# Kernel optimization log

Measured on AMD Instinct MI355X. Metric: run time of the kernel, lower is better.

## Reference

```python
import jax, jax.numpy as jnp
import numpy as np

N = 100000   # nodes
E = 1600000  # directed edges (avg degree 16)
D = 128      # num_feature == hidden_channels


def setup_inputs() -> dict:
    key = jax.random.key(0)
    ks = jax.random.split(key, 8)
    s = 1.0 / np.sqrt(D)
    x = jax.random.normal(ks[0], (N, D), jnp.float32)
    edge_index = jax.random.randint(ks[1], (2, E), 0, N, dtype=jnp.int32)
    W1 = jax.random.normal(ks[2], (D, D), jnp.float32) * s
    W2 = jax.random.normal(ks[3], (D, D), jnp.float32) * s
    W3 = jax.random.normal(ks[4], (D, D), jnp.float32) * s
    b1 = jnp.zeros((D,), jnp.float32)
    b2 = jnp.zeros((D,), jnp.float32)
    b3 = jnp.zeros((D,), jnp.float32)
    return {"x": x, "edge_index": edge_index, "W1": W1, "b1": b1,
            "W2": W2, "b2": b2, "W3": W3, "b3": b3}


def reference(x, edge_index, W1, b1, W2, b2, W3, b3):
    # GCNConv with added self-loops and symmetric normalization:
    #   out = D^{-1/2} (A + I) D^{-1/2} (x W) + b
    loops = jnp.arange(N, dtype=edge_index.dtype)
    src = jnp.concatenate([edge_index[0], loops])  # [E+N]
    dst = jnp.concatenate([edge_index[1], loops])
    deg = jax.ops.segment_sum(jnp.ones_like(dst, x.dtype), dst, num_segments=N)
    dinv = jax.lax.rsqrt(deg)                      # deg >= 1 (self-loops)
    norm = dinv[src] * dinv[dst]                   # [E+N]

    def conv(h, W, b):
        h = h @ W                                   # [N, D] dense GEMM
        msg = h[src] * norm[:, None]                # gather + scale [E+N, D]
        return jax.ops.segment_sum(msg, dst, num_segments=N) + b

    # dropout is identity in eval mode
    h = jax.nn.relu(conv(x, W1, b1))
    h = jax.nn.relu(conv(h, W2, b2))
    return conv(h, W3, b3)
```

## Files before the change

### kernel.cpp

```cpp
#include <hip/hip_runtime.h>
#include <hip/hip_fp16.h>

#define DFEAT 128
#define BNODES 256
#define BSHIFT 8
#define B1CHUNK 4096
#define SLABC 8192
#define TPB_TILES 2

typedef _Float16 f16x8 __attribute__((ext_vector_type(8)));
typedef _Float16 f16x4 __attribute__((ext_vector_type(4)));
typedef float f32x4 __attribute__((ext_vector_type(4)));


__global__ __launch_bounds__(256) void bin_k(const int* __restrict__ src, const int* __restrict__ dst,
                                             int* __restrict__ gcnt, unsigned int* __restrict__ slab,
                                             int E, int nbuck) {
    __shared__ int cnt[512];
    __shared__ int off[512];
    __shared__ int gbase[512];
    __shared__ int sd[256];
    __shared__ unsigned int buf[B1CHUNK];
    __shared__ unsigned short bid[B1CHUNK];
    int t = threadIdx.x;
    int base = blockIdx.x * B1CHUNK;
    int nloc = E - base;
    if (nloc > B1CHUNK) nloc = B1CHUNK;
    cnt[t] = 0;
    cnt[t + 256] = 0;
    __syncthreads();
    int k = t;
    for (; k + 768 < nloc; k += 1024) {
        int d0 = dst[base + k], d1 = dst[base + k + 256], d2 = dst[base + k + 512], d3 = dst[base + k + 768];
        atomicAdd(&cnt[d0 >> BSHIFT], 1);
        atomicAdd(&cnt[d1 >> BSHIFT], 1);
        atomicAdd(&cnt[d2 >> BSHIFT], 1);
        atomicAdd(&cnt[d3 >> BSHIFT], 1);
    }
    for (; k < nloc; k += 256) atomicAdd(&cnt[dst[base + k] >> BSHIFT], 1);
    __syncthreads();
    int v0 = cnt[2 * t], v1 = cnt[2 * t + 1];
    int tsum = v0 + v1;
    sd[t] = tsum;
    __syncthreads();
    for (int o = 1; o < 256; o <<= 1) {
        int x = (t >= o) ? sd[t - o] : 0;
        __syncthreads();
        sd[t] += x;
        __syncthreads();
    }
    int texcl = sd[t] - tsum;
    off[2 * t] = texcl;
    off[2 * t + 1] = texcl + v0;
    if (2 * t < nbuck && v0 > 0) gbase[2 * t] = atomicAdd(&gcnt[2 * t], v0);
    if (2 * t + 1 < nbuck && v1 > 0) gbase[2 * t + 1] = atomicAdd(&gcnt[2 * t + 1], v1);
    __syncthreads();
    k = t;
    for (; k + 768 < nloc; k += 1024) {
        int d0 = dst[base + k], d1 = dst[base + k + 256], d2 = dst[base + k + 512], d3 = dst[base + k + 768];
        int s0 = src[base + k], s1 = src[base + k + 256], s2 = src[base + k + 512], s3 = src[base + k + 768];
        int b0 = d0 >> BSHIFT, b1_ = d1 >> BSHIFT, b2_ = d2 >> BSHIFT, b3_ = d3 >> BSHIFT;
        int r0 = atomicAdd(&off[b0], 1); buf[r0] = ((unsigned)s0 << BSHIFT) | (unsigned)(d0 & (BNODES - 1)); bid[r0] = (unsigned short)b0;
        int r1 = atomicAdd(&off[b1_], 1); buf[r1] = ((unsigned)s1 << BSHIFT) | (unsigned)(d1 & (BNODES - 1)); bid[r1] = (unsigned short)b1_;
        int r2 = atomicAdd(&off[b2_], 1); buf[r2] = ((unsigned)s2 << BSHIFT) | (unsigned)(d2 & (BNODES - 1)); bid[r2] = (unsigned short)b2_;
        int r3 = atomicAdd(&off[b3_], 1); buf[r3] = ((unsigned)s3 << BSHIFT) | (unsigned)(d3 & (BNODES - 1)); bid[r3] = (unsigned short)b3_;
    }
    for (; k < nloc; k += 256) {
        int d = dst[base + k];
        int s = src[base + k];
        int b = d >> BSHIFT;
        int r = atomicAdd(&off[b], 1);
        buf[r] = ((unsigned)s << BSHIFT) | (unsigned)(d & (BNODES - 1));
        bid[r] = (unsigned short)b;
    }
    __syncthreads();
    k = t;
    for (; k + 768 < nloc; k += 1024) {
#pragma unroll
        for (int u = 0; u < 4; ++u) {
            int kk = k + u * 256;
            int b = bid[kk];
            int o0 = off[b] - cnt[b];
            int pos = gbase[b] + (kk - o0);
            if (pos < SLABC) slab[(size_t)b * SLABC + pos] = buf[kk];
        }
    }
    for (; k < nloc; k += 256) {
        int b = bid[k];
        int o0 = off[b] - cnt[b];
        int pos = gbase[b] + (k - o0);
        if (pos < SLABC) slab[(size_t)b * SLABC + pos] = buf[k];
    }
}

__global__ __launch_bounds__(256) void bucketAB_k(const unsigned int* __restrict__ slab,
                                                  const int* __restrict__ gcnt,
                                                  int* __restrict__ rp, float* __restrict__ dinv,
                                                  int* __restrict__ cols, int N, int nbuck) {
    __shared__ int cnt[256];
    __shared__ int cur[256];
    __shared__ int psum[256];
    __shared__ int outb[SLABC];
    int t = threadIdx.x;
    int b = blockIdx.x;
    int n0 = b << BSHIFT;
    int nn = N - n0;
    if (nn > BNODES) nn = BNODES;
    int ne_raw = gcnt[b];
    int ne = ne_raw > SLABC ? SLABC : ne_raw;
    const unsigned int* sl = slab + (size_t)b * SLABC;
    int part = 0;
    for (int i = t; i < b; i += 256) part += gcnt[i];
    psum[t] = part;
    cnt[t] = 0;
    __syncthreads();
    for (int o = 128; o > 0; o >>= 1) {
        if (t < o) psum[t] += psum[t + o];
        __syncthreads();
    }
    int base = psum[0];
    int k = t;
    for (; k + 768 < ne; k += 1024) {
        unsigned a0 = sl[k], a1 = sl[k + 256], a2 = sl[k + 512], a3 = sl[k + 768];
        atomicAdd(&cnt[a0 & (BNODES - 1)], 1);
        atomicAdd(&cnt[a1 & (BNODES - 1)], 1);
        atomicAdd(&cnt[a2 & (BNODES - 1)], 1);
        atomicAdd(&cnt[a3 & (BNODES - 1)], 1);
    }
    for (; k < ne; k += 256) atomicAdd(&cnt[sl[k] & (BNODES - 1)], 1);
    __syncthreads();
    int deg = cnt[t];
    for (int o = 1; o < 256; o <<= 1) {
        int x = (t >= o) ? cnt[t - o] : 0;
        __syncthreads();
        cnt[t] += x;
        __syncthreads();
    }
    int excl = cnt[t] - deg;
    if (t < nn) {
        rp[n0 + t] = base + excl;
        dinv[n0 + t] = rsqrtf((float)(deg + 1));
    }
    if (b == nbuck - 1 && t == 0) rp[N] = base + ne_raw;
    cur[t] = excl;
    __syncthreads();
    k = t;
    for (; k + 768 < ne; k += 1024) {
        unsigned a0 = sl[k], a1 = sl[k + 256], a2 = sl[k + 512], a3 = sl[k + 768];
        int p0 = atomicAdd(&cur[a0 & (BNODES - 1)], 1); outb[p0] = (int)(a0 >> BSHIFT);
        int p1 = atomicAdd(&cur[a1 & (BNODES - 1)], 1); outb[p1] = (int)(a1 >> BSHIFT);
        int p2 = atomicAdd(&cur[a2 & (BNODES - 1)], 1); outb[p2] = (int)(a2 >> BSHIFT);
        int p3 = atomicAdd(&cur[a3 & (BNODES - 1)], 1); outb[p3] = (int)(a3 >> BSHIFT);
    }
    for (; k < ne; k += 256) {
        unsigned a = sl[k];
        int p = atomicAdd(&cur[a & (BNODES - 1)], 1);
        outb[p] = (int)(a >> BSHIFT);
    }
    __syncthreads();
    k = t;
    for (; k + 768 < ne; k += 1024) {
        int o0 = outb[k], o1 = outb[k + 256], o2 = outb[k + 512], o3 = outb[k + 768];
        cols[base + k] = o0;
        cols[base + k + 256] = o1;
        cols[base + k + 512] = o2;
        cols[base + k + 768] = o3;
    }
    for (; k < ne; k += 256) cols[base + k] = outb[k];
}

__global__ __launch_bounds__(256) void packW_k(const float* __restrict__ W0, const float* __restrict__ W1,
                                               const float* __restrict__ W2,
                                               const float* __restrict__ b0, const float* __restrict__ b1,
                                               const float* __restrict__ b2,
                                               _Float16* __restrict__ wpk, float* __restrict__ bp,
                                               int* __restrict__ gcnt) {
    int idx = blockIdx.x * 256 + threadIdx.x;
    int layer = idx >> 14;
    int e = idx & 16383;
    int k = e >> 7;
    int nn = e & 127;
    const float* W = (layer == 0) ? W0 : ((layer == 1) ? W1 : W2);
    int ksrc = (layer == 0) ? k : (((k & 7) << 4) | (k >> 3));
    float v = W[ksrc * DFEAT + nn];
    int kc = k >> 5, quad = (k >> 3) & 3, j = k & 7;
    int ct = nn >> 4;
    int pos = ((ct * 4 + kc) * 64 + quad * 16 + (nn & 15)) * 8 + j;
    wpk[(size_t)layer * 16384 + pos] = (_Float16)v;
    if (idx < 384) {
        int l = idx >> 7, p = idx & 127;
        int c = ((p & 7) << 4) | (p >> 3);
        const float* bb = (l == 0) ? b0 : ((l == 1) ? b1 : b2);
        bp[l * 128 + p] = bb[c];
    }
    if (idx < 512) gcnt[idx] = 0;
}


__device__ inline f16x8 ldA8(const float* p) {
    float4 a = *(const float4*)p;
    float4 b = *(const float4*)(p + 4);
    return f16x8{(_Float16)a.x, (_Float16)a.y, (_Float16)a.z, (_Float16)a.w,
                 (_Float16)b.x, (_Float16)b.y, (_Float16)b.z, (_Float16)b.w};
}
__device__ inline f16x8 ldA8(const __half* p) { return *(const f16x8*)p; }
__device__ inline f16x8 zero8() {
    return f16x8{(_Float16)0.f, (_Float16)0.f, (_Float16)0.f, (_Float16)0.f,
                 (_Float16)0.f, (_Float16)0.f, (_Float16)0.f, (_Float16)0.f};
}

template <typename TIN>
__global__ __launch_bounds__(256) void gemmP_k(const TIN* __restrict__ A, const _Float16* __restrict__ wfrag,
                                               const float* __restrict__ dinv, __half* __restrict__ C,
                                               int n, int ntiles) {
    __shared__ _Float16 al[8192];
    __shared__ _Float16 wl[16384];
    const int tid = threadIdx.x;
    const int wv_ = tid >> 6;
    const int lane = tid & 63;
    const int t0 = blockIdx.x * TPB_TILES;
    const int chunk = tid & 15;
    const int rsub = tid >> 4;
    const int kcS = chunk >> 2, quadS = chunk & 3;
    const int swzS = (kcS << 1) ^ (quadS & 1);

    for (int c = tid; c < 2048; c += 256)
        *(f16x8*)&wl[c * 8] = *(const f16x8*)&wfrag[c * 8];

    f16x8 pre[4];
    {
        int row0 = t0 * 64;
#pragma unroll
        for (int p = 0; p < 4; ++p) {
            int gr = row0 + p * 16 + rsub;
            pre[p] = (gr < n) ? ldA8(&A[(size_t)gr * DFEAT + chunk * 8]) : zero8();
        }
    }
    for (int tt = 0; tt < TPB_TILES; ++tt) {
        int tile = t0 + tt;
        if (tile >= ntiles) break;
        int row0 = tile * 64;
#pragma unroll
        for (int p = 0; p < 4; ++p) {
            int idx = (p * 4 + kcS) * 64 + quadS * 16 + rsub;
            *(f16x8*)&al[(idx ^ swzS) * 8] = pre[p];
        }
        __syncthreads();
        if (tt + 1 < TPB_TILES && tile + 1 < ntiles) {
            int nrow0 = (tile + 1) * 64;
#pragma unroll
            for (int p = 0; p < 4; ++p) {
                int gr = nrow0 + p * 16 + rsub;
                pre[p] = (gr < n) ? ldA8(&A[(size_t)gr * DFEAT + chunk * 8]) : zero8();
            }
        }
        f16x8 af[4];
        const int swzR = (lane >> 4) & 1;
#pragma unroll
        for (int kc = 0; kc < 4; ++kc) {
            int idx = (wv_ * 4 + kc) * 64 + lane;
            af[kc] = *(f16x8*)&al[(idx ^ (kc << 1) ^ swzR) * 8];
        }
        const int quad = lane >> 4, cb = lane & 15;
        const int rbase = row0 + wv_ * 16 + quad * 4;
        float ds[4];
#pragma unroll
        for (int r = 0; r < 4; ++r) ds[r] = (rbase + r < n) ? dinv[rbase + r] : 0.f;
        f32x4 acc[8];
#pragma unroll
        for (int ct = 0; ct < 8; ++ct) acc[ct] = (f32x4){0.f, 0.f, 0.f, 0.f};
#pragma unroll
        for (int ct = 0; ct < 8; ++ct) {
#pragma unroll
            for (int kc = 0; kc < 4; ++kc) {
                f16x8 bf = *(f16x8*)&wl[((ct * 4 + kc) * 64 + lane) * 8];
                acc[ct] = __builtin_amdgcn_mfma_f32_16x16x32_f16(af[kc], bf, acc[ct], 0, 0, 0);
            }
        }
#pragma unroll
        for (int r = 0; r < 4; ++r) {
            int gr = rbase + r;
            if (gr < n) {
                f16x8 o;
#pragma unroll
                for (int ct = 0; ct < 8; ++ct) o[ct] = (_Float16)(acc[ct][r] * ds[r]);
                *(f16x8*)&C[(size_t)gr * DFEAT + cb * 8] = o;
            }
        }
        __syncthreads();
    }
}


__device__ inline float2 agg_row(const __half* __restrict__ T, const int* __restrict__ rowptr,
                                 const int* __restrict__ cols, int wid, int lane, int fb) {
    float2 t0 = __half22float2(*(const __half2*)(T + (size_t)wid * DFEAT + fb));
    float ax = t0.x;
    float ay = t0.y;
    int s = rowptr[wid], e = rowptr[wid + 1];
    for (int p = s; p < e; ) {
        int take = e - p;
        if (take > 64) take = 64;
        int q = p + lane;
        if (q >= e) q = e - 1;
        int ci = cols[q];
        int j = 0;
        for (; j + 8 <= take; j += 8) {
            int c0 = __builtin_amdgcn_readlane(ci, j + 0);
            int c1 = __builtin_amdgcn_readlane(ci, j + 1);
            int c2 = __builtin_amdgcn_readlane(ci, j + 2);
            int c3 = __builtin_amdgcn_readlane(ci, j + 3);
            int c4 = __builtin_amdgcn_readlane(ci, j + 4);
            int c5 = __builtin_amdgcn_readlane(ci, j + 5);
            int c6 = __builtin_amdgcn_readlane(ci, j + 6);
            int c7 = __builtin_amdgcn_readlane(ci, j + 7);
            float2 v0 = __half22float2(*(const __half2*)(T + (size_t)c0 * DFEAT + fb));
            float2 v1 = __half22float2(*(const __half2*)(T + (size_t)c1 * DFEAT + fb));
            float2 v2 = __half22float2(*(const __half2*)(T + (size_t)c2 * DFEAT + fb));
            float2 v3 = __half22float2(*(const __half2*)(T + (size_t)c3 * DFEAT + fb));
            float2 v4 = __half22float2(*(const __half2*)(T + (size_t)c4 * DFEAT + fb));
            float2 v5 = __half22float2(*(const __half2*)(T + (size_t)c5 * DFEAT + fb));
            float2 v6 = __half22float2(*(const __half2*)(T + (size_t)c6 * DFEAT + fb));
            float2 v7 = __half22float2(*(const __half2*)(T + (size_t)c7 * DFEAT + fb));
            ax += v0.x; ay += v0.y;
            ax += v1.x; ay += v1.y;
            ax += v2.x; ay += v2.y;
            ax += v3.x; ay += v3.y;
            ax += v4.x; ay += v4.y;
            ax += v5.x; ay += v5.y;
            ax += v6.x; ay += v6.y;
            ax += v7.x; ay += v7.y;
        }
        for (; j < take; ++j) {
            int c = __builtin_amdgcn_readlane(ci, j);
            float2 v = __half22float2(*(const __half2*)(T + (size_t)c * DFEAT + fb));
            ax += v.x; ay += v.y;
        }
        p += take;
    }
    return make_float2(ax, ay);
}

__global__ __launch_bounds__(256) void agg_k(const __half* __restrict__ T, const float* __restrict__ dinv,
                                             const int* __restrict__ rowptr, const int* __restrict__ cols,
                                             const float* __restrict__ biasp,
                                             __half* __restrict__ out, int n) {
    int wid = (int)((blockIdx.x * (size_t)blockDim.x + threadIdx.x) >> 6);
    int lane = threadIdx.x & 63;
    if (wid >= n) return;
    int fb = lane * 2;
    float2 a = agg_row(T, rowptr, cols, wid, lane, fb);
    float dw = dinv[wid];
    float ox = fmaxf(dw * a.x + biasp[fb], 0.f);
    float oy = fmaxf(dw * a.y + biasp[fb + 1], 0.f);
    *(__half2*)(out + (size_t)wid * DFEAT + fb) = __floats2half2_rn(ox, oy);
}

__global__ __launch_bounds__(256) void aggF_k(const __half* __restrict__ T, const float* __restrict__ dinv,
                                              const int* __restrict__ rowptr, const int* __restrict__ cols,
                                              const float* __restrict__ biasp,
                                              float* __restrict__ out, int n) {
    int wid = (int)((blockIdx.x * (size_t)blockDim.x + threadIdx.x) >> 6);
    int lane = threadIdx.x & 63;
    if (wid >= n) return;
    int fb = lane * 2;
    float2 a = agg_row(T, rowptr, cols, wid, lane, fb);
    float dw = dinv[wid];
    float ox = dw * a.x + biasp[fb];
    float oy = dw * a.y + biasp[fb + 1];
    int c0 = ((fb & 7) << 4) | (fb >> 3);
    int c1 = (((fb + 1) & 7) << 4) | ((fb + 1) >> 3);
    out[(size_t)wid * DFEAT + c0] = ox;
    out[(size_t)wid * DFEAT + c1] = oy;
}


extern "C" void kernel_launch(void* const* d_in, const int* in_sizes, int n_in,
                              void* d_out, int out_size, void* d_ws, size_t ws_size,
                              hipStream_t stream) {
    const float* x  = (const float*)d_in[0];
    const int*   ei = (const int*)d_in[1];
    const float* W1 = (const float*)d_in[2];
    const float* b1 = (const float*)d_in[3];
    const float* W2 = (const float*)d_in[4];
    const float* b2 = (const float*)d_in[5];
    const float* W3 = (const float*)d_in[6];
    const float* b3 = (const float*)d_in[7];
    float* out = (float*)d_out;

    const int N = in_sizes[0] / DFEAT;
    const int E = in_sizes[1] / 2;
    const int* srcp = ei;
    const int* dstp = ei + E;

    size_t off = 0;
    auto alloc = [&](size_t bytes) -> void* {
        void* p = (char*)d_ws + off;
        off += (bytes + 255) & ~(size_t)255;
        return p;
    };
    const int nbuck = (N + BNODES - 1) / BNODES;

    int*    gcnt = (int*)alloc(2048);
    int*    rp   = (int*)alloc((size_t)(N + 1) * 4);
    float*  dinv = (float*)alloc((size_t)N * 4);
    _Float16* wpk = (_Float16*)alloc((size_t)3 * 16384 * 2);
    float*  bp   = (float*)alloc(3 * 128 * 4);
    unsigned int* slab = (unsigned int*)alloc((size_t)nbuck * SLABC * 4);
    int*    cols = (int*)alloc((size_t)E * 4);
    __half* bufA = (__half*)alloc((size_t)N * DFEAT * 2);
    __half* bufB = (__half*)alloc((size_t)N * DFEAT * 2);

    packW_k<<<192, 256, 0, stream>>>(W1, W2, W3, b1, b2, b3, wpk, bp, gcnt);
    bin_k<<<(E + B1CHUNK - 1) / B1CHUNK, 256, 0, stream>>>(srcp, dstp, gcnt, slab, E, nbuck);
    bucketAB_k<<<nbuck, 256, 0, stream>>>(slab, gcnt, rp, dinv, cols, N, nbuck);

    int ntiles = (N + 63) / 64;
    int gemmGrid = (ntiles + TPB_TILES - 1) / TPB_TILES;
    int aggGrid  = (int)(((size_t)N * 64 + 255) / 256);

    gemmP_k<float><<<gemmGrid, 256, 0, stream>>>(x, wpk, dinv, bufA, N, ntiles);
    agg_k<<<aggGrid, 256, 0, stream>>>(bufA, dinv, rp, cols, bp, bufB, N);

    gemmP_k<__half><<<gemmGrid, 256, 0, stream>>>(bufB, wpk + 16384, dinv, bufA, N, ntiles);
    agg_k<<<aggGrid, 256, 0, stream>>>(bufA, dinv, rp, cols, bp + 128, bufB, N);

    gemmP_k<__half><<<gemmGrid, 256, 0, stream>>>(bufB, wpk + 32768, dinv, bufA, N, ntiles);
    aggF_k<<<aggGrid, 256, 0, stream>>>(bufA, dinv, rp, cols, bp + 256, out, N);
}
```

Baseline: 379.4 us.

## Fuse edge binning with first-layer GEMM and apply source norm during aggregation

The edge-binning kernel and the layer-1 dense GEMM now run in one launch, with block ranges split between the two jobs, so the GEMM work overlaps the atomic-heavy binning. This is possible because the first GEMM no longer scales rows by dinv, which is not yet computed at that point. A new aggregation kernel applies dinv of each source node per edge instead. The cost is an extra dinv gather per edge in the first aggregation, plus shared memory sized for the larger of the two roles.

```diff
diff --git a/kernel.cpp b/kernel.cpp
--- a/kernel.cpp
+++ b/kernel.cpp
@@ -7,167 +7,12 @@
 #define B1CHUNK 4096
 #define SLABC 8192
 #define TPB_TILES 2
+#define TPB1 2
 
 typedef _Float16 f16x8 __attribute__((ext_vector_type(8)));
 typedef _Float16 f16x4 __attribute__((ext_vector_type(4)));
 typedef float f32x4 __attribute__((ext_vector_type(4)));
 
-
-__global__ __launch_bounds__(256) void bin_k(const int* __restrict__ src, const int* __restrict__ dst,
-                                             int* __restrict__ gcnt, unsigned int* __restrict__ slab,
-                                             int E, int nbuck) {
-    __shared__ int cnt[512];
-    __shared__ int off[512];
-    __shared__ int gbase[512];
-    __shared__ int sd[256];
-    __shared__ unsigned int buf[B1CHUNK];
-    __shared__ unsigned short bid[B1CHUNK];
-    int t = threadIdx.x;
-    int base = blockIdx.x * B1CHUNK;
-    int nloc = E - base;
-    if (nloc > B1CHUNK) nloc = B1CHUNK;
-    cnt[t] = 0;
-    cnt[t + 256] = 0;
-    __syncthreads();
-    int k = t;
-    for (; k + 768 < nloc; k += 1024) {
-        int d0 = dst[base + k], d1 = dst[base + k + 256], d2 = dst[base + k + 512], d3 = dst[base + k + 768];
-        atomicAdd(&cnt[d0 >> BSHIFT], 1);
-        atomicAdd(&cnt[d1 >> BSHIFT], 1);
-        atomicAdd(&cnt[d2 >> BSHIFT], 1);
-        atomicAdd(&cnt[d3 >> BSHIFT], 1);
-    }
-    for (; k < nloc; k += 256) atomicAdd(&cnt[dst[base + k] >> BSHIFT], 1);
-    __syncthreads();
-    int v0 = cnt[2 * t], v1 = cnt[2 * t + 1];
-    int tsum = v0 + v1;
-    sd[t] = tsum;
-    __syncthreads();
-    for (int o = 1; o < 256; o <<= 1) {
-        int x = (t >= o) ? sd[t - o] : 0;
-        __syncthreads();
-        sd[t] += x;
-        __syncthreads();
-    }
-    int texcl = sd[t] - tsum;
-    off[2 * t] = texcl;
-    off[2 * t + 1] = texcl + v0;
-    if (2 * t < nbuck && v0 > 0) gbase[2 * t] = atomicAdd(&gcnt[2 * t], v0);
-    if (2 * t + 1 < nbuck && v1 > 0) gbase[2 * t + 1] = atomicAdd(&gcnt[2 * t + 1], v1);
-    __syncthreads();
-    k = t;
-    for (; k + 768 < nloc; k += 1024) {
-        int d0 = dst[base + k], d1 = dst[base + k + 256], d2 = dst[base + k + 512], d3 = dst[base + k + 768];
-        int s0 = src[base + k], s1 = src[base + k + 256], s2 = src[base + k + 512], s3 = src[base + k + 768];
-        int b0 = d0 >> BSHIFT, b1_ = d1 >> BSHIFT, b2_ = d2 >> BSHIFT, b3_ = d3 >> BSHIFT;
-        int r0 = atomicAdd(&off[b0], 1); buf[r0] = ((unsigned)s0 << BSHIFT) | (unsigned)(d0 & (BNODES - 1)); bid[r0] = (unsigned short)b0;
-        int r1 = atomicAdd(&off[b1_], 1); buf[r1] = ((unsigned)s1 << BSHIFT) | (unsigned)(d1 & (BNODES - 1)); bid[r1] = (unsigned short)b1_;
-        int r2 = atomicAdd(&off[b2_], 1); buf[r2] = ((unsigned)s2 << BSHIFT) | (unsigned)(d2 & (BNODES - 1)); bid[r2] = (unsigned short)b2_;
-        int r3 = atomicAdd(&off[b3_], 1); buf[r3] = ((unsigned)s3 << BSHIFT) | (unsigned)(d3 & (BNODES - 1)); bid[r3] = (unsigned short)b3_;
-    }
-    for (; k < nloc; k += 256) {
-        int d = dst[base + k];
-        int s = src[base + k];
-        int b = d >> BSHIFT;
-        int r = atomicAdd(&off[b], 1);
-        buf[r] = ((unsigned)s << BSHIFT) | (unsigned)(d & (BNODES - 1));
-        bid[r] = (unsigned short)b;
-    }
-    __syncthreads();
-    k = t;
-    for (; k + 768 < nloc; k += 1024) {
-#pragma unroll
-        for (int u = 0; u < 4; ++u) {
-            int kk = k + u * 256;
-            int b = bid[kk];
-            int o0 = off[b] - cnt[b];
-            int pos = gbase[b] + (kk - o0);
-            if (pos < SLABC) slab[(size_t)b * SLABC + pos] = buf[kk];
-        }
-    }
-    for (; k < nloc; k += 256) {
-        int b = bid[k];
-        int o0 = off[b] - cnt[b];
-        int pos = gbase[b] + (k - o0);
-        if (pos < SLABC) slab[(size_t)b * SLABC + pos] = buf[k];
-    }
-}
-
-__global__ __launch_bounds__(256) void bucketAB_k(const unsigned int* __restrict__ slab,
-                                                  const int* __restrict__ gcnt,
-                                                  int* __restrict__ rp, float* __restrict__ dinv,
-                                                  int* __restrict__ cols, int N, int nbuck) {
-    __shared__ int cnt[256];
-    __shared__ int cur[256];
-    __shared__ int psum[256];
-    __shared__ int outb[SLABC];
-    int t = threadIdx.x;
-    int b = blockIdx.x;
-    int n0 = b << BSHIFT;
-    int nn = N - n0;
-    if (nn > BNODES) nn = BNODES;
-    int ne_raw = gcnt[b];
-    int ne = ne_raw > SLABC ? SLABC : ne_raw;
-    const unsigned int* sl = slab + (size_t)b * SLABC;
-    int part = 0;
-    for (int i = t; i < b; i += 256) part += gcnt[i];
-    psum[t] = part;
-    cnt[t] = 0;
-    __syncthreads();
-    for (int o = 128; o > 0; o >>= 1) {
-        if (t < o) psum[t] += psum[t + o];
-        __syncthreads();
-    }
-    int base = psum[0];
-    int k = t;
-    for (; k + 768 < ne; k += 1024) {
-        unsigned a0 = sl[k], a1 = sl[k + 256], a2 = sl[k + 512], a3 = sl[k + 768];
-        atomicAdd(&cnt[a0 & (BNODES - 1)], 1);
-        atomicAdd(&cnt[a1 & (BNODES - 1)], 1);
-        atomicAdd(&cnt[a2 & (BNODES - 1)], 1);
-        atomicAdd(&cnt[a3 & (BNODES - 1)], 1);
-    }
-    for (; k < ne; k += 256) atomicAdd(&cnt[sl[k] & (BNODES - 1)], 1);
-    __syncthreads();
-    int deg = cnt[t];
-    for (int o = 1; o < 256; o <<= 1) {
-        int x = (t >= o) ? cnt[t - o] : 0;
-        __syncthreads();
-        cnt[t] += x;
-        __syncthreads();
-    }
-    int excl = cnt[t] - deg;
-    if (t < nn) {
-        rp[n0 + t] = base + excl;
-        dinv[n0 + t] = rsqrtf((float)(deg + 1));
-    }
-    if (b == nbuck - 1 && t == 0) rp[N] = base + ne_raw;
-    cur[t] = excl;
-    __syncthreads();
-    k = t;
-    for (; k + 768 < ne; k += 1024) {
-        unsigned a0 = sl[k], a1 = sl[k + 256], a2 = sl[k + 512], a3 = sl[k + 768];
-        int p0 = atomicAdd(&cur[a0 & (BNODES - 1)], 1); outb[p0] = (int)(a0 >> BSHIFT);
-        int p1 = atomicAdd(&cur[a1 & (BNODES - 1)], 1); outb[p1] = (int)(a1 >> BSHIFT);
-        int p2 = atomicAdd(&cur[a2 & (BNODES - 1)], 1); outb[p2] = (int)(a2 >> BSHIFT);
-        int p3 = atomicAdd(&cur[a3 & (BNODES - 1)], 1); outb[p3] = (int)(a3 >> BSHIFT);
-    }
-    for (; k < ne; k += 256) {
-        unsigned a = sl[k];
-        int p = atomicAdd(&cur[a & (BNODES - 1)], 1);
-        outb[p] = (int)(a >> BSHIFT);
-    }
-    __syncthreads();
-    k = t;
-    for (; k + 768 < ne; k += 1024) {
-        int o0 = outb[k], o1 = outb[k + 256], o2 = outb[k + 512], o3 = outb[k + 768];
-        cols[base + k] = o0;
-        cols[base + k + 256] = o1;
-        cols[base + k + 512] = o2;
-        cols[base + k + 768] = o3;
-    }
-    for (; k < ne; k += 256) cols[base + k] = outb[k];
-}
 
 __global__ __launch_bounds__(256) void packW_k(const float* __restrict__ W0, const float* __restrict__ W1,
                                                const float* __restrict__ W2,
@@ -196,7 +41,6 @@
     if (idx < 512) gcnt[idx] = 0;
 }
 
-
 __device__ inline f16x8 ldA8(const float* p) {
     float4 a = *(const float4*)p;
     float4 b = *(const float4*)(p + 4);
@@ -207,6 +51,221 @@
 __device__ inline f16x8 zero8() {
     return f16x8{(_Float16)0.f, (_Float16)0.f, (_Float16)0.f, (_Float16)0.f,
                  (_Float16)0.f, (_Float16)0.f, (_Float16)0.f, (_Float16)0.f};
+}
+
+struct BinSh {
+    int cnt[512];
+    int off[512];
+    int gbase[512];
+    int sd[256];
+    unsigned int buf[B1CHUNK];
+    unsigned short bid[B1CHUNK];
+};
+struct G1Sh {
+    _Float16 wl[16384];
+};
+
+__global__ __launch_bounds__(256) void binGemm1_k(const int* __restrict__ src, const int* __restrict__ dst,
+                                                  int* __restrict__ gcnt, unsigned int* __restrict__ slab,
+                                                  int E, int nbuck, int nbin,
+                                                  const float* __restrict__ A, const _Float16* __restrict__ wfrag,
+                                                  __half* __restrict__ C, int n, int ntiles) {
+    __shared__ __align__(16) char smem[32768];
+    int t = threadIdx.x;
+    if (blockIdx.x >= nbin) {
+        _Float16* wl = ((G1Sh*)smem)->wl;
+        const int wv_ = t >> 6;
+        const int lane = t & 63;
+        const int m = lane & 15;
+        const int q = lane >> 4;
+        for (int c = t; c < 2048; c += 256)
+            *(f16x8*)&wl[c * 8] = *(const f16x8*)&wfrag[c * 8];
+        __syncthreads();
+        int t0 = (blockIdx.x - nbin) * TPB1;
+        int tend = t0 + TPB1;
+        if (tend > ntiles) tend = ntiles;
+        for (int tile = t0; tile < tend; ++tile) {
+            int row0 = tile * 64;
+            int ga = row0 + wv_ * 16 + m;
+            f16x8 af[4];
+            if (ga < n) {
+#pragma unroll
+                for (int kc = 0; kc < 4; ++kc)
+                    af[kc] = ldA8(&A[(size_t)ga * DFEAT + kc * 32 + q * 8]);
+            } else {
+#pragma unroll
+                for (int kc = 0; kc < 4; ++kc) af[kc] = zero8();
+            }
+            f32x4 acc[8];
+#pragma unroll
+            for (int ct = 0; ct < 8; ++ct) acc[ct] = (f32x4){0.f, 0.f, 0.f, 0.f};
+#pragma unroll
+            for (int ct = 0; ct < 8; ++ct) {
+#pragma unroll
+                for (int kc = 0; kc < 4; ++kc) {
+                    f16x8 bf = *(f16x8*)&wl[((ct * 4 + kc) * 64 + lane) * 8];
+                    acc[ct] = __builtin_amdgcn_mfma_f32_16x16x32_f16(af[kc], bf, acc[ct], 0, 0, 0);
+                }
+            }
+            const int rbase = row0 + wv_ * 16 + q * 4;
+#pragma unroll
+            for (int r = 0; r < 4; ++r) {
+                int gr = rbase + r;
+                if (gr < n) {
+                    f16x8 o;
+#pragma unroll
+                    for (int ct = 0; ct < 8; ++ct) o[ct] = (_Float16)acc[ct][r];
+                    *(f16x8*)&C[(size_t)gr * DFEAT + m * 8] = o;
+                }
+            }
+        }
+        return;
+    }
+    BinSh* B = (BinSh*)smem;
+    int base = blockIdx.x * B1CHUNK;
+    int nloc = E - base;
+    if (nloc > B1CHUNK) nloc = B1CHUNK;
+    B->cnt[t] = 0;
+    B->cnt[t + 256] = 0;
+    __syncthreads();
+    int k = t;
+    for (; k + 768 < nloc; k += 1024) {
+        int d0 = dst[base + k], d1 = dst[base + k + 256], d2 = dst[base + k + 512], d3 = dst[base + k + 768];
+        atomicAdd(&B->cnt[d0 >> BSHIFT], 1);
+        atomicAdd(&B->cnt[d1 >> BSHIFT], 1);
+        atomicAdd(&B->cnt[d2 >> BSHIFT], 1);
+        atomicAdd(&B->cnt[d3 >> BSHIFT], 1);
+    }
+    for (; k < nloc; k += 256) atomicAdd(&B->cnt[dst[base + k] >> BSHIFT], 1);
+    __syncthreads();
+    int v0 = B->cnt[2 * t], v1 = B->cnt[2 * t + 1];
+    int tsum = v0 + v1;
+    B->sd[t] = tsum;
+    __syncthreads();
+    for (int o = 1; o < 256; o <<= 1) {
+        int x = (t >= o) ? B->sd[t - o] : 0;
+        __syncthreads();
+        B->sd[t] += x;
+        __syncthreads();
+    }
+    int texcl = B->sd[t] - tsum;
+    B->off[2 * t] = texcl;
+    B->off[2 * t + 1] = texcl + v0;
+    if (2 * t < nbuck && v0 > 0) B->gbase[2 * t] = atomicAdd(&gcnt[2 * t], v0);
+    if (2 * t + 1 < nbuck && v1 > 0) B->gbase[2 * t + 1] = atomicAdd(&gcnt[2 * t + 1], v1);
+    __syncthreads();
+    k = t;
+    for (; k + 768 < nloc; k += 1024) {
+        int d0 = dst[base + k], d1 = dst[base + k + 256], d2 = dst[base + k + 512], d3 = dst[base + k + 768];
+        int s0 = src[base + k], s1 = src[base + k + 256], s2 = src[base + k + 512], s3 = src[base + k + 768];
+        int b0_ = d0 >> BSHIFT, b1_ = d1 >> BSHIFT, b2_ = d2 >> BSHIFT, b3_ = d3 >> BSHIFT;
+        int r0 = atomicAdd(&B->off[b0_], 1); B->buf[r0] = ((unsigned)s0 << BSHIFT) | (unsigned)(d0 & (BNODES - 1)); B->bid[r0] = (unsigned short)b0_;
+        int r1 = atomicAdd(&B->off[b1_], 1); B->buf[r1] = ((unsigned)s1 << BSHIFT) | (unsigned)(d1 & (BNODES - 1)); B->bid[r1] = (unsigned short)b1_;
+        int r2 = atomicAdd(&B->off[b2_], 1); B->buf[r2] = ((unsigned)s2 << BSHIFT) | (unsigned)(d2 & (BNODES - 1)); B->bid[r2] = (unsigned short)b2_;
+        int r3 = atomicAdd(&B->off[b3_], 1); B->buf[r3] = ((unsigned)s3 << BSHIFT) | (unsigned)(d3 & (BNODES - 1)); B->bid[r3] = (unsigned short)b3_;
+    }
+    for (; k < nloc; k += 256) {
+        int d = dst[base + k];
+        int s = src[base + k];
+        int b = d >> BSHIFT;
+        int r = atomicAdd(&B->off[b], 1);
+        B->buf[r] = ((unsigned)s << BSHIFT) | (unsigned)(d & (BNODES - 1));
+        B->bid[r] = (unsigned short)b;
+    }
+    __syncthreads();
+    k = t;
+    for (; k + 768 < nloc; k += 1024) {
+#pragma unroll
+        for (int u = 0; u < 4; ++u) {
+            int kk = k + u * 256;
+            int b = B->bid[kk];
+            int o0 = B->off[b] - B->cnt[b];
+            int pos = B->gbase[b] + (kk - o0);
+            if (pos < SLABC) slab[(size_t)b * SLABC + pos] = B->buf[kk];
+        }
+    }
+    for (; k < nloc; k += 256) {
+        int b = B->bid[k];
+        int o0 = B->off[b] - B->cnt[b];
+        int pos = B->gbase[b] + (k - o0);
+        if (pos < SLABC) slab[(size_t)b * SLABC + pos] = B->buf[k];
+    }
+}
+
+__global__ __launch_bounds__(256) void bucketAB_k(const unsigned int* __restrict__ slab,
+                                                  const int* __restrict__ gcnt,
+                                                  int* __restrict__ rp, float* __restrict__ dinv,
+                                                  int* __restrict__ cols, int N, int nbuck) {
+    __shared__ int cnt[256];
+    __shared__ int cur[256];
+    __shared__ int psum[256];
+    __shared__ int outb[SLABC];
+    int t = threadIdx.x;
+    int b = blockIdx.x;
+    int n0 = b << BSHIFT;
+    int nn = N - n0;
+    if (nn > BNODES) nn = BNODES;
+    int ne_raw = gcnt[b];
+    int ne = ne_raw > SLABC ? SLABC : ne_raw;
+    const unsigned int* sl = slab + (size_t)b * SLABC;
+    int part = 0;
+    for (int i = t; i < b; i += 256) part += gcnt[i];
+    psum[t] = part;
+    cnt[t] = 0;
+    __syncthreads();
+    for (int o = 128; o > 0; o >>= 1) {
+        if (t < o) psum[t] += psum[t + o];
+        __syncthreads();
+    }
+    int base = psum[0];
+    int k = t;
+    for (; k + 768 < ne; k += 1024) {
+        unsigned a0 = sl[k], a1 = sl[k + 256], a2 = sl[k + 512], a3 = sl[k + 768];
+        atomicAdd(&cnt[a0 & (BNODES - 1)], 1);
+        atomicAdd(&cnt[a1 & (BNODES - 1)], 1);
+        atomicAdd(&cnt[a2 & (BNODES - 1)], 1);
+        atomicAdd(&cnt[a3 & (BNODES - 1)], 1);
+    }
+    for (; k < ne; k += 256) atomicAdd(&cnt[sl[k] & (BNODES - 1)], 1);
+    __syncthreads();
+    int deg = cnt[t];
+    for (int o = 1; o < 256; o <<= 1) {
+        int x = (t >= o) ? cnt[t - o] : 0;
+        __syncthreads();
+        cnt[t] += x;
+        __syncthreads();
+    }
+    int excl = cnt[t] - deg;
+    if (t < nn) {
+        rp[n0 + t] = base + excl;
+        dinv[n0 + t] = rsqrtf((float)(deg + 1));
+    }
+    if (b == nbuck - 1 && t == 0) rp[N] = base + ne_raw;
+    cur[t] = excl;
+    __syncthreads();
+    k = t;
+    for (; k + 768 < ne; k += 1024) {
+        unsigned a0 = sl[k], a1 = sl[k + 256], a2 = sl[k + 512], a3 = sl[k + 768];
+        int p0 = atomicAdd(&cur[a0 & (BNODES - 1)], 1); outb[p0] = (int)(a0 >> BSHIFT);
+        int p1 = atomicAdd(&cur[a1 & (BNODES - 1)], 1); outb[p1] = (int)(a1 >> BSHIFT);
+        int p2 = atomicAdd(&cur[a2 & (BNODES - 1)], 1); outb[p2] = (int)(a2 >> BSHIFT);
+        int p3 = atomicAdd(&cur[a3 & (BNODES - 1)], 1); outb[p3] = (int)(a3 >> BSHIFT);
+    }
+    for (; k < ne; k += 256) {
+        unsigned a = sl[k];
+        int p = atomicAdd(&cur[a & (BNODES - 1)], 1);
+        outb[p] = (int)(a >> BSHIFT);
+    }
+    __syncthreads();
+    k = t;
+    for (; k + 768 < ne; k += 1024) {
+        int o0 = outb[k], o1 = outb[k + 256], o2 = outb[k + 512], o3 = outb[k + 768];
+        cols[base + k] = o0;
+        cols[base + k + 256] = o1;
+        cols[base + k + 512] = o2;
+        cols[base + k + 768] = o3;
+    }
+    for (; k < ne; k += 256) cols[base + k] = outb[k];
 }
 
 template <typename TIN>
@@ -291,6 +350,67 @@
     }
 }
 
+
+__global__ __launch_bounds__(256) void aggW_k(const __half* __restrict__ T, const float* __restrict__ dinv,
+                                              const int* __restrict__ rowptr, const int* __restrict__ cols,
+                                              const float* __restrict__ biasp,
+                                              __half* __restrict__ out, int n) {
+    int wid = (int)((blockIdx.x * (size_t)blockDim.x + threadIdx.x) >> 6);
+    int lane = threadIdx.x & 63;
+    if (wid >= n) return;
+    int fb = lane * 2;
+    float di = dinv[wid];
+    float2 t0 = __half22float2(*(const __half2*)(T + (size_t)wid * DFEAT + fb));
+    float ax = di * t0.x;
+    float ay = di * t0.y;
+    int s = rowptr[wid], e = rowptr[wid + 1];
+    for (int p = s; p < e; ) {
+        int take = e - p;
+        if (take > 64) take = 64;
+        int q = p + lane;
+        if (q >= e) q = e - 1;
+        int ci = cols[q];
+        int j = 0;
+        for (; j + 8 <= take; j += 8) {
+            int c0 = __builtin_amdgcn_readlane(ci, j + 0);
+            int c1 = __builtin_amdgcn_readlane(ci, j + 1);
+            int c2 = __builtin_amdgcn_readlane(ci, j + 2);
+            int c3 = __builtin_amdgcn_readlane(ci, j + 3);
+            int c4 = __builtin_amdgcn_readlane(ci, j + 4);
+            int c5 = __builtin_amdgcn_readlane(ci, j + 5);
+            int c6 = __builtin_amdgcn_readlane(ci, j + 6);
+            int c7 = __builtin_amdgcn_readlane(ci, j + 7);
+            float w0 = dinv[c0], w1 = dinv[c1], w2 = dinv[c2], w3 = dinv[c3];
+            float w4 = dinv[c4], w5 = dinv[c5], w6 = dinv[c6], w7 = dinv[c7];
+            float2 v0 = __half22float2(*(const __half2*)(T + (size_t)c0 * DFEAT + fb));
+            float2 v1 = __half22float2(*(const __half2*)(T + (size_t)c1 * DFEAT + fb));
+            float2 v2 = __half22float2(*(const __half2*)(T + (size_t)c2 * DFEAT + fb));
+            float2 v3 = __half22float2(*(const __half2*)(T + (size_t)c3 * DFEAT + fb));
+            float2 v4 = __half22float2(*(const __half2*)(T + (size_t)c4 * DFEAT + fb));
+            float2 v5 = __half22float2(*(const __half2*)(T + (size_t)c5 * DFEAT + fb));
+            float2 v6 = __half22float2(*(const __half2*)(T + (size_t)c6 * DFEAT + fb));
+            float2 v7 = __half22float2(*(const __half2*)(T + (size_t)c7 * DFEAT + fb));
+            ax += w0 * v0.x; ay += w0 * v0.y;
+            ax += w1 * v1.x; ay += w1 * v1.y;
+            ax += w2 * v2.x; ay += w2 * v2.y;
+            ax += w3 * v3.x; ay += w3 * v3.y;
+            ax += w4 * v4.x; ay += w4 * v4.y;
+            ax += w5 * v5.x; ay += w5 * v5.y;
+            ax += w6 * v6.x; ay += w6 * v6.y;
+            ax += w7 * v7.x; ay += w7 * v7.y;
+        }
+        for (; j < take; ++j) {
+            int c = __builtin_amdgcn_readlane(ci, j);
+            float w = dinv[c];
+            float2 v = __half22float2(*(const __half2*)(T + (size_t)c * DFEAT + fb));
+            ax += w * v.x; ay += w * v.y;
+        }
+        p += take;
+    }
+    float ox = fmaxf(di * ax + biasp[fb], 0.f);
+    float oy = fmaxf(di * ay + biasp[fb + 1], 0.f);
+    *(__half2*)(out + (size_t)wid * DFEAT + fb) = __floats2half2_rn(ox, oy);
+}
 
 __device__ inline float2 agg_row(const __half* __restrict__ T, const int* __restrict__ rowptr,
                                  const int* __restrict__ cols, int wid, int lane, int fb) {
@@ -411,16 +531,18 @@
     __half* bufA = (__half*)alloc((size_t)N * DFEAT * 2);
     __half* bufB = (__half*)alloc((size_t)N * DFEAT * 2);
 
-    packW_k<<<192, 256, 0, stream>>>(W1, W2, W3, b1, b2, b3, wpk, bp, gcnt);
-    bin_k<<<(E + B1CHUNK - 1) / B1CHUNK, 256, 0, stream>>>(srcp, dstp, gcnt, slab, E, nbuck);
-    bucketAB_k<<<nbuck, 256, 0, stream>>>(slab, gcnt, rp, dinv, cols, N, nbuck);
-
+    const int nbin = (E + B1CHUNK - 1) / B1CHUNK;
     int ntiles = (N + 63) / 64;
+    int g1blocks = (ntiles + TPB1 - 1) / TPB1;
     int gemmGrid = (ntiles + TPB_TILES - 1) / TPB_TILES;
     int aggGrid  = (int)(((size_t)N * 64 + 255) / 256);
 
-    gemmP_k<float><<<gemmGrid, 256, 0, stream>>>(x, wpk, dinv, bufA, N, ntiles);
-    agg_k<<<aggGrid, 256, 0, stream>>>(bufA, dinv, rp, cols, bp, bufB, N);
+    packW_k<<<192, 256, 0, stream>>>(W1, W2, W3, b1, b2, b3, wpk, bp, gcnt);
+    binGemm1_k<<<nbin + g1blocks, 256, 0, stream>>>(srcp, dstp, gcnt, slab, E, nbuck, nbin,
+                                                    x, wpk, bufA, N, ntiles);
+    bucketAB_k<<<nbuck, 256, 0, stream>>>(slab, gcnt, rp, dinv, cols, N, nbuck);
+
+    aggW_k<<<aggGrid, 256, 0, stream>>>(bufA, dinv, rp, cols, bp, bufB, N);
 
     gemmP_k<__half><<<gemmGrid, 256, 0, stream>>>(bufB, wpk + 16384, dinv, bufA, N, ntiles);
     agg_k<<<aggGrid, 256, 0, stream>>>(bufA, dinv, rp, cols, bp + 128, bufB, N);
```

Result: no change. 378.5 us (median of 2 runs) (-0.2%).
